# Optimization experiments

Hardware: AMD Instinct MI355X
Metric: run time of the kernel (lower is better)

The kernel has to match this reference:

```python
import jax, jax.numpy as jnp
import numpy as np

N = 50000      # nodes
E = 800000     # edges (avg degree 16)
H = 256        # h_size
MAXCTX = 8     # max_context


def setup_inputs() -> dict:
    key = jax.random.key(0)
    ks = jax.random.split(key, 6)
    x = jax.random.normal(ks[0], (N, H), jnp.float32)
    edge_index = jax.random.randint(ks[1], (2, E), 0, N)
    node_label = jax.random.randint(ks[2], (N, MAXCTX), 0, N)
    context_len = jax.random.randint(ks[3], (N,), 0, MAXCTX)
    gcn_W = jax.random.normal(ks[4], (H, H), jnp.float32) / np.sqrt(H)
    gcn_b = jnp.zeros((H,), jnp.float32)
    resize_W = jax.random.normal(ks[5], (H * MAXCTX, H), jnp.float32) / np.sqrt(H * MAXCTX)
    resize_b = jnp.zeros((H,), jnp.float32)
    return {"x": x, "edge_index": edge_index, "node_label": node_label,
            "context_len": context_len, "gcn_W": gcn_W, "gcn_b": gcn_b,
            "resize_W": resize_W, "resize_b": resize_b}


def gcn_conv(x, edge_index, W, b, n):
    # PyG GCNConv: add self-loops, symmetric deg^-1/2 normalization, then linear.
    loop = jnp.arange(n)
    src = jnp.concatenate([edge_index[0], loop])
    dst = jnp.concatenate([edge_index[1], loop])
    deg = jax.ops.segment_sum(jnp.ones_like(dst, x.dtype), dst, num_segments=n)
    inv_sqrt = jax.lax.rsqrt(jnp.maximum(deg, 1.0))  # deg>=1 due to self-loops
    h = x @ W                                        # [n, H]
    coef = inv_sqrt[src] * inv_sqrt[dst]             # [E+n]
    out = jax.ops.segment_sum(h[src] * coef[:, None], dst, num_segments=n)
    return out + b


def reference(x, edge_index, node_label, context_len, gcn_W, gcn_b, resize_W, resize_b):
    n = x.shape[0]
    # gcn_layers=2: relu(GCN(x)) (dropout is identity in eval) then GCN again.
    feat = jax.nn.relu(gcn_conv(x, edge_index, gcn_W, gcn_b, n))
    feat = gcn_conv(feat, edge_index, gcn_W, gcn_b, n)
    # Batched variable-length context gather with zero padding.
    ctx = feat[node_label]                                            # [n, MAXCTX, H]
    mask = (jnp.arange(node_label.shape[1])[None, :] < context_len[:, None])
    ctx = ctx * mask[:, :, None].astype(feat.dtype)
    ctx = ctx.reshape(n, -1) @ resize_W + resize_b                    # [n, H]
    return feat * ctx                                                 # rep_vec per node
```

## Files before the change

kernel.cpp:

```cpp
#include <hip/hip_runtime.h>

typedef _Float16 f16;
typedef _Float16 f16x8 __attribute__((ext_vector_type(8)));
typedef float f32x16 __attribute__((ext_vector_type(16)));

#define MFMA(a, b, c) __builtin_amdgcn_mfma_f32_32x32x16_f16(a, b, c, 0, 0, 0)

__device__ __forceinline__ void gload_lds16(const f16* g, f16* l) {
    __builtin_amdgcn_global_load_lds(
        (const __attribute__((address_space(1))) unsigned int*)g,
        (__attribute__((address_space(3))) unsigned int*)l, 16, 0, 0);
}


#define NBMAX 256
#define CHUNK 8192
#define CAP   8192

__global__ __launch_bounds__(256) void bin_count_trans(
        const int* __restrict__ dst, const int* __restrict__ clen,
        int* __restrict__ gbc, int* __restrict__ ghist, int E, int n, int chn,
        int nbc,
        const float* __restrict__ gW, f16* __restrict__ Wth, f16* __restrict__ Wtl,
        const float* __restrict__ rW, f16* __restrict__ Rth, f16* __restrict__ Rtl) {
    __shared__ int bc[NBMAX];
    __shared__ int ch[9];
    __shared__ f16 Th[64][68], Tl[64][68];
    int tid = threadIdx.x;
    if ((int)blockIdx.x >= nbc) {
        int b = (int)blockIdx.x - nbc;
        const float* src; f16 *dh, *dl; int K, k0, n0;
        if (b < 128) { src = rW; dh = Rth; dl = Rtl; K = 2048; k0 = (b >> 2) * 64; n0 = (b & 3) * 64; }
        else { int bb = b - 128; src = gW; dh = Wth; dl = Wtl; K = 256; k0 = (bb >> 2) * 64; n0 = (bb & 3) * 64; }
        int c = tid & 63, r0 = tid >> 6;
        for (int rr = r0; rr < 64; rr += 4) {
            float v = src[(size_t)(k0 + rr) * 256 + n0 + c];
            f16 h = (f16)v;
            Th[rr][c] = h; Tl[rr][c] = (f16)(v - (float)h);
        }
        __syncthreads();
        int k = tid & 63, nr0 = tid >> 6;
        for (int nn = nr0; nn < 64; nn += 4) {
            size_t oidx = (size_t)(n0 + nn) * K + k0 + k;
            dh[oidx] = Th[k][nn];
            dl[oidx] = Tl[k][nn];
        }
        return;
    }
    bc[tid] = 0;
    if (tid < 9) ch[tid] = 0;
    __syncthreads();
    int e0 = blockIdx.x * CHUNK, e1 = min(e0 + CHUNK, E);
    for (int i = e0 + tid; i < e1; i += 256)
        atomicAdd(&bc[dst[i] >> 8], 1);
    int n0 = blockIdx.x * chn, n1 = min(n0 + chn, n);
    for (int i = n0 + tid; i < n1; i += 256) {
        int l = clen[i]; l = max(0, min(8, l));
        atomicAdd(&ch[l], 1);
    }
    __syncthreads();
    if (bc[tid]) atomicAdd(&gbc[tid], bc[tid]);
    if (tid < 9 && ch[tid]) atomicAdd(&ghist[tid], ch[tid]);
}

__global__ __launch_bounds__(256) void scan_small(
        const int* __restrict__ gbc, int* __restrict__ gbase,
        const int* __restrict__ ghist, int* __restrict__ chbase, int nb, int E) {
    __shared__ int s[NBMAX];
    int tid = threadIdx.x;
    int v = (tid < nb) ? gbc[tid] : 0;
    s[tid] = v;
    __syncthreads();
    for (int off = 1; off < 256; off <<= 1) {
        int u = (tid >= off) ? s[tid - off] : 0;
        __syncthreads();
        s[tid] += u;
        __syncthreads();
    }
    if (tid <= nb) gbase[tid] = (tid < nb) ? s[tid] - v : E;
    if (tid == 0) {
        int run = 0;
        for (int i = 0; i < 9; ++i) { int c = ghist[i]; chbase[i] = run; run += c; }
    }
}

__global__ __launch_bounds__(256) void bin_scatter(
        const int* __restrict__ src, const int* __restrict__ dst,
        const int* __restrict__ clen,
        const int* __restrict__ gbase, int* __restrict__ gfill,
        const int* __restrict__ chbase, int* __restrict__ chfill,
        int2* __restrict__ binned, int* __restrict__ perm, int* __restrict__ plen,
        int E, int n, int chn) {
    __shared__ int bc[NBMAX], bb[NBMAX];
    __shared__ int cc[9], cb[9];
    int tid = threadIdx.x;
    bc[tid] = 0;
    if (tid < 9) cc[tid] = 0;
    __syncthreads();
    int e0 = blockIdx.x * CHUNK, e1 = min(e0 + CHUNK, E);
    for (int i = e0 + tid; i < e1; i += 256)
        atomicAdd(&bc[dst[i] >> 8], 1);
    int n0 = blockIdx.x * chn, n1 = min(n0 + chn, n);
    for (int i = n0 + tid; i < n1; i += 256) {
        int l = clen[i]; l = max(0, min(8, l));
        atomicAdd(&cc[l], 1);
    }
    __syncthreads();
    {
        int c = bc[tid];
        bb[tid] = c ? gbase[tid] + atomicAdd(&gfill[tid], c) : 0;
        bc[tid] = 0;
    }
    if (tid < 9) {
        int c = cc[tid];
        cb[tid] = c ? chbase[tid] + atomicAdd(&chfill[tid], c) : 0;
        cc[tid] = 0;
    }
    __syncthreads();
    for (int i = e0 + tid; i < e1; i += 256) {
        int d = dst[i], b = d >> 8;
        int p = bb[b] + atomicAdd(&bc[b], 1);
        binned[p] = make_int2(src[i], d);
    }
    for (int i = n0 + tid; i < n1; i += 256) {
        int l = clen[i]; l = max(0, min(8, l));
        int p = cb[l] + atomicAdd(&cc[l], 1);
        perm[p] = i;
        plen[p] = l;
    }
}

__global__ __launch_bounds__(256) void csr_build(
        const int2* __restrict__ binned, const int* __restrict__ gbase,
        int* __restrict__ row_ptr, float* __restrict__ inv_s,
        int* __restrict__ ew, int E, int n) {
    __shared__ int cnt[256], base[256], fill[256];
    __shared__ int ebuf[CAP];
    int tid = threadIdx.x, b = blockIdx.x;
    int e0 = gbase[b], e1 = gbase[b + 1], sz = e1 - e0;
    cnt[tid] = 0;
    __syncthreads();
    for (int i = e0 + tid; i < e1; i += 256)
        atomicAdd(&cnt[binned[i].y & 255], 1);
    __syncthreads();
    int v = cnt[tid];
    base[tid] = v;
    __syncthreads();
    for (int off = 1; off < 256; off <<= 1) {
        int u = (tid >= off) ? base[tid - off] : 0;
        __syncthreads();
        base[tid] += u;
        __syncthreads();
    }
    int ex = base[tid] - v;
    base[tid] = ex;
    fill[tid] = 0;
    int node = b * 256 + tid;
    if (node < n) {
        row_ptr[node] = e0 + ex;
        inv_s[node] = rsqrtf((float)(v + 1));
    }
    if (b == 0 && tid == 0) row_ptr[n] = E;
    __syncthreads();
    for (int i = e0 + tid; i < e1; i += 256) {
        int2 q = binned[i];
        int lo = q.y & 255;
        int p = base[lo] + atomicAdd(&fill[lo], 1);
        if (p < CAP) ebuf[p] = q.x; else ew[e0 + p] = q.x;
    }
    __syncthreads();
    int lim = min(sz, CAP);
    for (int p = tid; p < lim; p += 256) ew[e0 + p] = ebuf[p];
}


union H4 { f16 f[4]; ushort4 u; };

__global__ __launch_bounds__(512, 4) void agg_split(const float* __restrict__ X,
        const int* __restrict__ ew, const int* __restrict__ rp,
        const float* __restrict__ invs, f16* __restrict__ ohi, f16* __restrict__ olo, int n) {
    __shared__ float part[4][256];
    int w = threadIdx.x >> 6, lane = threadIdx.x & 63;
    int local = w >> 1, half = w & 1;
    int node = blockIdx.x * 4 + local;
    bool active = node < n;
    float4 acc = make_float4(0.f, 0.f, 0.f, 0.f);
    float si = 0.f;
    if (active) {
        si = invs[node];
        int e0 = rp[node], e1 = rp[node + 1];
        int mid = e0 + ((e1 - e0 + 1) >> 1);
        int lo = half ? mid : e0;
        int hi = half ? e1 : mid;
        if (!half) {
            float4 a = *((const float4*)(X + (size_t)node * 256) + lane);
            acc = make_float4(a.x * si, a.y * si, a.z * si, a.w * si);
        }
        int e = lo;
        for (; e + 8 <= hi; e += 8) {
            int q[8]; float ws[8]; float4 v[8];
            #pragma unroll
            for (int u = 0; u < 8; ++u) q[u] = ew[e + u];
            #pragma unroll
            for (int u = 0; u < 8; ++u) ws[u] = invs[q[u]];
            #pragma unroll
            for (int u = 0; u < 8; ++u) v[u] = *((const float4*)(X + (size_t)q[u] * 256) + lane);
            #pragma unroll
            for (int u = 0; u < 8; ++u) {
                acc.x = fmaf(ws[u], v[u].x, acc.x); acc.y = fmaf(ws[u], v[u].y, acc.y);
                acc.z = fmaf(ws[u], v[u].z, acc.z); acc.w = fmaf(ws[u], v[u].w, acc.w);
            }
        }
        for (; e < hi; ++e) {
            int q = ew[e];
            float wq = invs[q];
            float4 v = *((const float4*)(X + (size_t)q * 256) + lane);
            acc.x = fmaf(wq, v.x, acc.x); acc.y = fmaf(wq, v.y, acc.y);
            acc.z = fmaf(wq, v.z, acc.z); acc.w = fmaf(wq, v.w, acc.w);
        }
    }
    if (half) *(float4*)&part[local][lane * 4] = acc;
    __syncthreads();
    if (!half && active) {
        float4 o = *(const float4*)&part[local][lane * 4];
        float v0 = si * (acc.x + o.x), v1 = si * (acc.y + o.y);
        float v2 = si * (acc.z + o.z), v3 = si * (acc.w + o.w);
        H4 hh, ll;
        f16 h;
        h = (f16)v0; hh.f[0] = h; ll.f[0] = (f16)(v0 - (float)h);
        h = (f16)v1; hh.f[1] = h; ll.f[1] = (f16)(v1 - (float)h);
        h = (f16)v2; hh.f[2] = h; ll.f[2] = (f16)(v2 - (float)h);
        h = (f16)v3; hh.f[3] = h; ll.f[3] = (f16)(v3 - (float)h);
        size_t off = (size_t)node * 256 + lane * 4;
        *(ushort4*)(ohi + off) = hh.u;
        *(ushort4*)(olo + off) = ll.u;
    }
}


__global__ __launch_bounds__(256, 3) void gemm_lds(
        const f16* __restrict__ Ahi, const f16* __restrict__ Alo,
        const f16* __restrict__ Wth, const f16* __restrict__ Wtl,
        const float* __restrict__ bias,
        float* __restrict__ Of32, f16* __restrict__ Ohi, f16* __restrict__ Olo,
        int M, int relu) {
    __shared__ __align__(16) f16 LA[3][2][4096];
    int tid = threadIdx.x, w = tid >> 6, lane = tid & 63;
    int row0 = (int)blockIdx.x * 64;
    int m = lane & 31, kh = lane >> 5;
    const int T = 4;

    f32x16 acc[2][2] = {};

    {
        #define STAGE(t_, b_)                                                     \
        {                                                                         \
            int k0e_ = (t_) * 64;                                                 \
            int rl_ = lane >> 3;                                                  \
            int k8s_ = (lane & 7) ^ rl_;                                          \
            _Pragma("unroll")                                                     \
            for (int q = 0; q < 4; ++q) {                                         \
                int o_ = w * 4 + q;                                               \
                int mat_ = o_ >> 3, rg_ = o_ & 7;                                 \
                int r_ = row0 + rg_ * 8 + rl_;                                    \
                if (r_ >= M) r_ = M - 1;                                          \
                const f16* base_ = mat_ ? Alo : Ahi;                              \
                const f16* g_ = base_ + (size_t)r_ * 256 + k0e_ + k8s_ * 8;       \
                gload_lds16(g_, &LA[b_][mat_][rg_ * 512]);                        \
            }                                                                     \
        }
        STAGE(0, 0);
        STAGE(1, 1);
        asm volatile("s_waitcnt vmcnt(0)" ::: "memory");
        __builtin_amdgcn_s_barrier();
        __builtin_amdgcn_sched_barrier(0);
        for (int t = 0; t < T; ++t) {
            int b = t % 3;
            int k0e = t * 64;
            f16x8 Bh[4][2], Bl[4][2];
            #pragma unroll
            for (int jt = 0; jt < 2; ++jt) {
                int nn = w * 64 + jt * 32 + m;
                size_t boff = (size_t)nn * 256 + k0e + kh * 8;
                const f16* ph = Wth + boff;
                const f16* pl = Wtl + boff;
                #pragma unroll
                for (int s = 0; s < 4; ++s) {
                    Bh[s][jt] = *(const f16x8*)(ph + s * 16);
                    Bl[s][jt] = *(const f16x8*)(pl + s * 16);
                }
            }
            __builtin_amdgcn_sched_barrier(0);
            if (t + 2 < T) STAGE(t + 2, (t + 2) % 3);
            __builtin_amdgcn_sched_barrier(0);
            #pragma unroll
            for (int s = 0; s < 4; ++s) {
                int k8 = s * 2 + kh;
                int slot = (k8 ^ (m & 7)) * 8;
                f16x8 ah[2], al[2];
                #pragma unroll
                for (int i = 0; i < 2; ++i) {
                    int ro = (i * 32 + m) * 64;
                    ah[i] = *(const f16x8*)&LA[b][0][ro + slot];
                    al[i] = *(const f16x8*)&LA[b][1][ro + slot];
                }
                #pragma unroll
                for (int jt = 0; jt < 2; ++jt) {
                    #pragma unroll
                    for (int i = 0; i < 2; ++i) {
                        acc[i][jt] = MFMA(ah[i], Bh[s][jt], acc[i][jt]);
                        acc[i][jt] = MFMA(ah[i], Bl[s][jt], acc[i][jt]);
                        acc[i][jt] = MFMA(al[i], Bh[s][jt], acc[i][jt]);
                    }
                }
            }
            if (t + 2 < T) {
                asm volatile("s_waitcnt vmcnt(4)" ::: "memory");
            } else {
                asm volatile("s_waitcnt vmcnt(0)" ::: "memory");
            }
            __builtin_amdgcn_s_barrier();
            __builtin_amdgcn_sched_barrier(0);
        }
        #undef STAGE
    }

    #pragma unroll
    for (int jt = 0; jt < 2; ++jt) {
        int col = w * 64 + jt * 32 + m;
        float bv = bias[col];
        #pragma unroll
        for (int i = 0; i < 2; ++i) {
            #pragma unroll
            for (int r = 0; r < 16; ++r) {
                int row = row0 + i * 32 + (r & 3) + 8 * (r >> 2) + 4 * kh;
                if (row < M) {
                    float v = acc[i][jt][r] + bv;
                    if (relu) v = fmaxf(v, 0.f);
                    size_t idx = (size_t)row * 256 + col;
                    if (Of32) Of32[idx] = v;
                    if (Ohi) {
                        f16 h = (f16)v;
                        Ohi[idx] = h; Olo[idx] = (f16)(v - (float)h);
                    }
                }
            }
        }
    }
}


__global__ __launch_bounds__(256, 3) void ctx_gemm(
        const f16* __restrict__ fhi, const f16* __restrict__ flo,
        const int* __restrict__ perm, const int* __restrict__ plen,
        const int* __restrict__ label,
        const f16* __restrict__ Rth, const f16* __restrict__ Rtl,
        const float* __restrict__ rbias, float* __restrict__ out,
        const f16* __restrict__ zp, int M) {
    __shared__ __align__(16) f16 LA[3][2][4096];
    __shared__ int s_lbl[8][64];
    __shared__ int s_perm[64];
    __shared__ int s_max;
    int tid = threadIdx.x, w = tid >> 6, lane = tid & 63;
    int row0 = (int)(gridDim.x - 1 - blockIdx.x) * 64;
    int m = lane & 31, kh = lane >> 5;

    if (tid == 0) s_max = 0;
    __syncthreads();
    if (tid < 64) {
        int r = row0 + tid;
        int p = (r < M) ? perm[r] : -1;
        s_perm[tid] = p;
        int len = (r < M) ? plen[r] : 0;
        atomicMax(&s_max, len);
        int4 l0 = make_int4(-1, -1, -1, -1), l1 = l0;
        if (p >= 0) {
            l0 = *(const int4*)(label + (size_t)p * 8);
            l1 = *(const int4*)(label + (size_t)p * 8 + 4);
        }
        s_lbl[0][tid] = (0 < len) ? l0.x : -1;
        s_lbl[1][tid] = (1 < len) ? l0.y : -1;
        s_lbl[2][tid] = (2 < len) ? l0.z : -1;
        s_lbl[3][tid] = (3 < len) ? l0.w : -1;
        s_lbl[4][tid] = (4 < len) ? l1.x : -1;
        s_lbl[5][tid] = (5 < len) ? l1.y : -1;
        s_lbl[6][tid] = (6 < len) ? l1.z : -1;
        s_lbl[7][tid] = (7 < len) ? l1.w : -1;
    }
    __syncthreads();
    int T = s_max * 4;

    f32x16 acc[2][2] = {};

    if (T > 0) {
        #define STAGE(t_, b_)                                                     \
        {                                                                         \
            int j_ = (t_) >> 2, k0e_ = ((t_) & 3) * 64;                           \
            int rl_ = lane >> 3;                                                  \
            int k8s_ = (lane & 7) ^ rl_;                                          \
            _Pragma("unroll")                                                     \
            for (int q = 0; q < 4; ++q) {                                         \
                int o_ = w * 4 + q;                                               \
                int mat_ = o_ >> 3, rg_ = o_ & 7;                                 \
                int lbl_ = s_lbl[j_][rg_ * 8 + rl_];                              \
                const f16* base_ = mat_ ? flo : fhi;                              \
                const f16* g_ = (lbl_ >= 0)                                       \
                    ? base_ + (size_t)lbl_ * 256 + k0e_ + k8s_ * 8 : zp;          \
                gload_lds16(g_, &LA[b_][mat_][rg_ * 512]);                        \
            }                                                                     \
        }
        STAGE(0, 0);
        if (T > 1) STAGE(1, 1);
        asm volatile("s_waitcnt vmcnt(0)" ::: "memory");
        __builtin_amdgcn_s_barrier();
        __builtin_amdgcn_sched_barrier(0);
        for (int t = 0; t < T; ++t) {
            int b = t % 3;
            int j = t >> 2, k0e = (t & 3) * 64;
            f16x8 Bh[4][2], Bl[4][2];
            #pragma unroll
            for (int jt = 0; jt < 2; ++jt) {
                int nn = w * 64 + jt * 32 + m;
                size_t boff = (size_t)nn * 2048 + j * 256 + k0e + kh * 8;
                const f16* ph = Rth + boff;
                const f16* pl = Rtl + boff;
                #pragma unroll
                for (int s = 0; s < 4; ++s) {
                    Bh[s][jt] = *(const f16x8*)(ph + s * 16);
                    Bl[s][jt] = *(const f16x8*)(pl + s * 16);
                }
            }
            __builtin_amdgcn_sched_barrier(0);
            if (t + 2 < T) STAGE(t + 2, (t + 2) % 3);
            __builtin_amdgcn_sched_barrier(0);
            #pragma unroll
            for (int s = 0; s < 4; ++s) {
                int k8 = s * 2 + kh;
                int slot = (k8 ^ (m & 7)) * 8;
                f16x8 ah[2], al[2];
                #pragma unroll
                for (int i = 0; i < 2; ++i) {
                    int ro = (i * 32 + m) * 64;
                    ah[i] = *(const f16x8*)&LA[b][0][ro + slot];
                    al[i] = *(const f16x8*)&LA[b][1][ro + slot];
                }
                #pragma unroll
                for (int jt = 0; jt < 2; ++jt) {
                    #pragma unroll
                    for (int i = 0; i < 2; ++i) {
                        acc[i][jt] = MFMA(ah[i], Bh[s][jt], acc[i][jt]);
                        acc[i][jt] = MFMA(ah[i], Bl[s][jt], acc[i][jt]);
                        acc[i][jt] = MFMA(al[i], Bh[s][jt], acc[i][jt]);
                    }
                }
            }
            if (t + 2 < T) {
                asm volatile("s_waitcnt vmcnt(4)" ::: "memory");
            } else {
                asm volatile("s_waitcnt vmcnt(0)" ::: "memory");
            }
            __builtin_amdgcn_s_barrier();
            __builtin_amdgcn_sched_barrier(0);
        }
        #undef STAGE
    }

    #pragma unroll
    for (int jt = 0; jt < 2; ++jt) {
        int col = w * 64 + jt * 32 + m;
        float rbv = rbias[col];
        #pragma unroll
        for (int i = 0; i < 2; ++i) {
            #pragma unroll
            for (int r = 0; r < 16; ++r) {
                int lr = i * 32 + (r & 3) + 8 * (r >> 2) + 4 * kh;
                int p = s_perm[lr];
                if (p >= 0) {
                    size_t idx = (size_t)p * 256 + col;
                    float f2 = (float)fhi[idx] + (float)flo[idx];
                    out[idx] = f2 * (acc[i][jt][r] + rbv);
                }
            }
        }
    }
}


extern "C" void kernel_launch(void* const* d_in, const int* in_sizes, int n_in,
                              void* d_out, int out_size, void* d_ws, size_t ws_size,
                              hipStream_t stream) {
    const float* x    = (const float*)d_in[0];
    const int*   edge = (const int*)d_in[1];
    const int*   lbl  = (const int*)d_in[2];
    const int*   clen = (const int*)d_in[3];
    const float* gW   = (const float*)d_in[4];
    const float* gb   = (const float*)d_in[5];
    const float* rW   = (const float*)d_in[6];
    const float* rb   = (const float*)d_in[7];

    const int N = in_sizes[3];
    const int E = in_sizes[1] / 2;

    char* ws = (char*)d_ws;
    size_t off = 0;
    auto take = [&](size_t bytes) -> char* {
        char* p = ws + off;
        off = (off + bytes + 255) & ~(size_t)255;
        return p;
    };
    int*   g_small  = (int*)take(1024 * sizeof(int));
    int*   g_bcnt   = g_small;
    int*   g_bbase  = g_small + 256;
    int*   g_bfill  = g_small + 520;
    int*   g_chist  = g_small + 776;
    int*   g_chbase = g_small + 792;
    int*   g_chfill = g_small + 808;
    int*   row_ptr = (int*)take((size_t)(N + 1) * sizeof(int));
    int*   ew      = (int*)take((size_t)E * sizeof(int));
    int*   perm    = (int*)take((size_t)N * sizeof(int));
    int*   plen    = (int*)take((size_t)N * sizeof(int));
    float* inv_s   = (float*)take((size_t)N * sizeof(float));
    f16*   zp      = (f16*)take(1024);
    f16*   Wth     = (f16*)take((size_t)256 * 256 * sizeof(f16));
    f16*   Wtl     = (f16*)take((size_t)256 * 256 * sizeof(f16));
    f16*   Rth     = (f16*)take((size_t)256 * 2048 * sizeof(f16));
    f16*   Rtl     = (f16*)take((size_t)256 * 2048 * sizeof(f16));
    f16*   Ahi     = (f16*)take((size_t)N * 256 * sizeof(f16));
    f16*   Alo     = (f16*)take((size_t)N * 256 * sizeof(f16));
    float* Y1      = (float*)take((size_t)N * 256 * sizeof(float));
    f16*   Fhi     = (f16*)take((size_t)N * 256 * sizeof(f16));
    f16*   Flo     = (f16*)take((size_t)N * 256 * sizeof(f16));
    int2*  binned  = (int2*)Y1;

    hipMemsetAsync(g_small, 0, 1024 * sizeof(int), stream);
    hipMemsetAsync(zp, 0, 1024, stream);

    int NB   = (N + 255) >> 8;
    int GBIN = (E + CHUNK - 1) / CHUNK;
    int CHN  = (N + GBIN - 1) / GBIN;

    bin_count_trans<<<GBIN + 144, 256, 0, stream>>>(edge + E, clen, g_bcnt, g_chist,
                                                    E, N, CHN, GBIN,
                                                    gW, Wth, Wtl, rW, Rth, Rtl);
    scan_small<<<1, 256, 0, stream>>>(g_bcnt, g_bbase, g_chist, g_chbase, NB, E);
    bin_scatter<<<GBIN, 256, 0, stream>>>(edge, edge + E, clen, g_bbase, g_bfill,
                                          g_chbase, g_chfill, binned, perm, plen,
                                          E, N, CHN);
    csr_build<<<NB, 256, 0, stream>>>(binned, g_bbase, row_ptr, inv_s, ew, E, N);

    int gB64 = (N + 63) / 64;
    agg_split<<<(N + 3) / 4, 512, 0, stream>>>(x, ew, row_ptr, inv_s, Ahi, Alo, N);
    gemm_lds<<<gB64, 256, 0, stream>>>(Ahi, Alo, Wth, Wtl, gb, Y1, nullptr, nullptr, N, 1);
    agg_split<<<(N + 3) / 4, 512, 0, stream>>>(Y1, ew, row_ptr, inv_s, Ahi, Alo, N);
    gemm_lds<<<gB64, 256, 0, stream>>>(Ahi, Alo, Wth, Wtl, gb, nullptr, Fhi, Flo, N, 0);
    ctx_gemm<<<gB64, 256, 0, stream>>>(Fhi, Flo, perm, plen, lbl, Rth, Rtl,
                                       rb, (float*)d_out, zp, N);
}
```

Measured before the change: 670.7 us.

## Split ctx_gemm across 8 waves with double-buffered staging

The context GEMM kernel now runs 512 threads per block, so each wave owns 32 output columns instead of 64. That halves per-wave accumulator and B-fragment register use. The triple-buffered LDS pipeline with explicit vmcnt waits becomes a simpler double buffer with __syncthreads. B fragments are now loaded inline per k-step rather than prefetched ahead of staging, which trades less latency hiding for more waves per block and less register pressure.

Measured after the change: 670.7 us (median of 2 runs). About the same (+0.0%).

```diff
diff --git a/kernel.cpp b/kernel.cpp
--- a/kernel.cpp
+++ b/kernel.cpp
@@ -350,14 +350,14 @@
 }
 
 
-__global__ __launch_bounds__(256, 3) void ctx_gemm(
+__global__ __launch_bounds__(512) void ctx_gemm(
         const f16* __restrict__ fhi, const f16* __restrict__ flo,
         const int* __restrict__ perm, const int* __restrict__ plen,
         const int* __restrict__ label,
         const f16* __restrict__ Rth, const f16* __restrict__ Rtl,
         const float* __restrict__ rbias, float* __restrict__ out,
         const f16* __restrict__ zp, int M) {
-    __shared__ __align__(16) f16 LA[3][2][4096];
+    __shared__ __align__(16) f16 LA[2][2][4096];
     __shared__ int s_lbl[8][64];
     __shared__ int s_perm[64];
     __shared__ int s_max;
@@ -390,7 +390,7 @@
     __syncthreads();
     int T = s_max * 4;
 
-    f32x16 acc[2][2] = {};
+    f32x16 acc[2] = {};
 
     if (T > 0) {
         #define STAGE(t_, b_)                                                     \
@@ -399,8 +399,8 @@
             int rl_ = lane >> 3;                                                  \
             int k8s_ = (lane & 7) ^ rl_;                                          \
             _Pragma("unroll")                                                     \
-            for (int q = 0; q < 4; ++q) {                                         \
-                int o_ = w * 4 + q;                                               \
+            for (int q = 0; q < 2; ++q) {                                         \
+                int o_ = w * 2 + q;                                               \
                 int mat_ = o_ >> 3, rg_ = o_ & 7;                                 \
                 int lbl_ = s_lbl[j_][rg_ * 8 + rl_];                              \
                 const f16* base_ = mat_ ? flo : fhi;                              \
@@ -410,29 +410,15 @@
             }                                                                     \
         }
         STAGE(0, 0);
-        if (T > 1) STAGE(1, 1);
-        asm volatile("s_waitcnt vmcnt(0)" ::: "memory");
-        __builtin_amdgcn_s_barrier();
-        __builtin_amdgcn_sched_barrier(0);
+        __syncthreads();
         for (int t = 0; t < T; ++t) {
-            int b = t % 3;
+            if (t + 1 < T) STAGE(t + 1, (t + 1) & 1);
+            int b = t & 1;
             int j = t >> 2, k0e = (t & 3) * 64;
-            f16x8 Bh[4][2], Bl[4][2];
-            #pragma unroll
-            for (int jt = 0; jt < 2; ++jt) {
-                int nn = w * 64 + jt * 32 + m;
-                size_t boff = (size_t)nn * 2048 + j * 256 + k0e + kh * 8;
-                const f16* ph = Rth + boff;
-                const f16* pl = Rtl + boff;
-                #pragma unroll
-                for (int s = 0; s < 4; ++s) {
-                    Bh[s][jt] = *(const f16x8*)(ph + s * 16);
-                    Bl[s][jt] = *(const f16x8*)(pl + s * 16);
-                }
-            }
-            __builtin_amdgcn_sched_barrier(0);
-            if (t + 2 < T) STAGE(t + 2, (t + 2) % 3);
-            __builtin_amdgcn_sched_barrier(0);
+            int nn = w * 32 + m;
+            size_t boff = (size_t)nn * 2048 + j * 256 + k0e + kh * 8;
+            const f16* pBh = Rth + boff;
+            const f16* pBl = Rtl + boff;
             #pragma unroll
             for (int s = 0; s < 4; ++s) {
                 int k8 = s * 2 + kh;
@@ -444,30 +430,22 @@
                     ah[i] = *(const f16x8*)&LA[b][0][ro + slot];
                     al[i] = *(const f16x8*)&LA[b][1][ro + slot];
                 }
+                f16x8 bh = *(const f16x8*)(pBh + s * 16);
+                f16x8 bl = *(const f16x8*)(pBl + s * 16);
                 #pragma unroll
-                for (int jt = 0; jt < 2; ++jt) {
-                    #pragma unroll
-                    for (int i = 0; i < 2; ++i) {
-                        acc[i][jt] = MFMA(ah[i], Bh[s][jt], acc[i][jt]);
-                        acc[i][jt] = MFMA(ah[i], Bl[s][jt], acc[i][jt]);
-                        acc[i][jt] = MFMA(al[i], Bh[s][jt], acc[i][jt]);
-                    }
-                }
-            }
-            if (t + 2 < T) {
-                asm volatile("s_waitcnt vmcnt(4)" ::: "memory");
-            } else {
-                asm volatile("s_waitcnt vmcnt(0)" ::: "memory");
-            }
-            __builtin_amdgcn_s_barrier();
-            __builtin_amdgcn_sched_barrier(0);
+                for (int i = 0; i < 2; ++i) {
+                    acc[i] = MFMA(ah[i], bh, acc[i]);
+                    acc[i] = MFMA(ah[i], bl, acc[i]);
+                    acc[i] = MFMA(al[i], bh, acc[i]);
+                }
+            }
+            __syncthreads();
         }
         #undef STAGE
     }
 
-    #pragma unroll
-    for (int jt = 0; jt < 2; ++jt) {
-        int col = w * 64 + jt * 32 + m;
+    {
+        int col = w * 32 + m;
         float rbv = rbias[col];
         #pragma unroll
         for (int i = 0; i < 2; ++i) {
@@ -478,7 +456,7 @@
                 if (p >= 0) {
                     size_t idx = (size_t)p * 256 + col;
                     float f2 = (float)fhi[idx] + (float)flo[idx];
-                    out[idx] = f2 * (acc[i][jt][r] + rbv);
+                    out[idx] = f2 * (acc[i][r] + rbv);
                 }
             }
         }
@@ -553,6 +531,6 @@
     gemm_lds<<<gB64, 256, 0, stream>>>(Ahi, Alo, Wth, Wtl, gb, Y1, nullptr, nullptr, N, 1);
     agg_split<<<(N + 3) / 4, 512, 0, stream>>>(Y1, ew, row_ptr, inv_s, Ahi, Alo, N);
     gemm_lds<<<gB64, 256, 0, stream>>>(Ahi, Alo, Wth, Wtl, gb, nullptr, Fhi, Flo, N, 0);
-    ctx_gemm<<<gB64, 256, 0, stream>>>(Fhi, Flo, perm, plen, lbl, Rth, Rtl,
+    ctx_gemm<<<gB64, 512, 0, stream>>>(Fhi, Flo, perm, plen, lbl, Rth, Rtl,
                                        rb, (float*)d_out, zp, N);
 }
```
